# Kernel optimization log

Hardware: AMD Instinct MI355X
Metric: run time of the kernel (lower is better)

## Reference

```python
import jax, jax.numpy as jnp
import numpy as np
import math

EMBED_DIM = 1024
NUM_HEADS = 16
HEAD_DIM = EMBED_DIM // NUM_HEADS
B, S = 4, 2048


def setup_inputs() -> dict:
    key = jax.random.key(0)
    ks = jax.random.split(key, 12)
    sc = 1.0 / math.sqrt(EMBED_DIM)
    inp = {
        'query': jax.random.normal(ks[0], (B, S, EMBED_DIM), jnp.float32),
        'key': jax.random.normal(ks[1], (B, S, EMBED_DIM), jnp.float32),
        'value': jax.random.normal(ks[2], (B, S, EMBED_DIM), jnp.float32),
        # causal mask: 1 = attend, 0 = masked (matches masked_fill(attn_mask == 0, -inf))
        'attn_mask': jnp.tril(jnp.ones((S, S), jnp.int32)),
        'Wq': jax.random.normal(ks[3], (EMBED_DIM, EMBED_DIM), jnp.float32) * sc,
        'bq': jax.random.normal(ks[4], (EMBED_DIM,), jnp.float32) * sc,
        'Wk': jax.random.normal(ks[5], (EMBED_DIM, EMBED_DIM), jnp.float32) * sc,
        'bk': jax.random.normal(ks[6], (EMBED_DIM,), jnp.float32) * sc,
        'Wv': jax.random.normal(ks[7], (EMBED_DIM, EMBED_DIM), jnp.float32) * sc,
        'bv': jax.random.normal(ks[8], (EMBED_DIM,), jnp.float32) * sc,
        'Wo': jax.random.normal(ks[9], (EMBED_DIM, EMBED_DIM), jnp.float32) * sc,
        'bo': jax.random.normal(ks[10], (EMBED_DIM,), jnp.float32) * sc,
    }
    return inp


def reference(query, key, value, attn_mask, Wq, bq, Wk, bk, Wv, bv, Wo, bo):
    b, s, _ = query.shape
    # torch nn.Linear: x @ W.T + b
    q = (query @ Wq.T + bq).reshape(b, s, NUM_HEADS, HEAD_DIM)
    k = (key @ Wk.T + bk).reshape(b, s, NUM_HEADS, HEAD_DIM)
    v = (value @ Wv.T + bv).reshape(b, s, NUM_HEADS, HEAD_DIM)
    scores = jnp.einsum('bqhd,bkhd->bhqk', q, k) / math.sqrt(HEAD_DIM)
    neg_inf = jnp.asarray(-jnp.inf, scores.dtype)
    scores = jnp.where(attn_mask[None, None, :, :] == 0, neg_inf, scores)
    attn = jax.nn.softmax(scores, axis=-1)
    # dropout is identity in eval mode
    out = jnp.einsum('bhqk,bkhd->bqhd', attn, v).reshape(b, s, EMBED_DIM)
    return out @ Wo.T + bo
```

## Files before the change

kernel.cpp:

```cpp
#include <hip/hip_runtime.h>
#include <math.h>


#define EMBED 1024
#define SEQ   2048
#define NH    16
#define HD    64
#define QSCALE 0.18033688011112042f

typedef __attribute__((ext_vector_type(4))) float f32x4;
typedef __attribute__((ext_vector_type(8))) short s16x8;
typedef __attribute__((ext_vector_type(4))) short s16x4;
typedef __attribute__((ext_vector_type(4))) unsigned int u32x4;
typedef __attribute__((ext_vector_type(2))) unsigned int u32x2;

#define GLDS16(gp, lp) __builtin_amdgcn_global_load_lds( \
    (const __attribute__((address_space(1))) void*)(gp), \
    (__attribute__((address_space(3))) void*)(lp), 16, 0, 0)

__device__ __forceinline__ unsigned short f2bf(float f) {
    unsigned int u = __builtin_bit_cast(unsigned int, f);
    u += 0x7fffu + ((u >> 16) & 1u);
    return (unsigned short)(u >> 16);
}
__device__ __forceinline__ unsigned int pkbf(float lo, float hi) {
    return __builtin_amdgcn_perm(__builtin_bit_cast(unsigned int, hi),
                                 __builtin_bit_cast(unsigned int, lo),
                                 0x07060302u);
}

struct CvtArgs { const float* s[4]; unsigned short* d[4]; };
__global__ void cvt_w(CvtArgs ca)
{
    const float* in = ca.s[blockIdx.y];
    unsigned short* out = ca.d[blockIdx.y];
    int i = blockIdx.x * 256 + threadIdx.x;
    f32x4 v = *(const f32x4*)(in + (size_t)i * 4);
    s16x4 p;
    p[0] = (short)f2bf(v[0]); p[1] = (short)f2bf(v[1]);
    p[2] = (short)f2bf(v[2]); p[3] = (short)f2bf(v[3]);
    *(s16x4*)(out + (size_t)i * 4) = p;
}

struct ProjArgs {
    const float* X[3];
    const unsigned short* W[3];
    const float* Bz[3];
    unsigned short* Oz[3];
};
__global__ void __launch_bounds__(256)
gemm_qkv(ProjArgs pa)
{
    __shared__ float Af[128 * 64];
    __shared__ unsigned short Bb[128 * 64];
    const int z = blockIdx.z;
    const float* X = pa.X[z];
    const unsigned short* Wb = pa.W[z];
    const float* bias = pa.Bz[z];
    unsigned short* Out = pa.Oz[z];
    const float scale = (z == 0) ? QSCALE : 1.0f;
    const int tid = threadIdx.x, lane = tid & 63, wv = tid >> 6;
    const int g = lane >> 4, c = lane & 15;
    const int wx = wv & 1, wy = wv >> 1;
    const int bm0 = blockIdx.x * 128, bn0 = blockIdx.y * 128;

    f32x4 acc[4][4];
#pragma unroll
    for (int i = 0; i < 4; ++i)
#pragma unroll
        for (int n = 0; n < 4; ++n) acc[i][n] = f32x4{0.f, 0.f, 0.f, 0.f};

    for (int k0 = 0; k0 < EMBED; k0 += 64) {
        __syncthreads();
#pragma unroll
        for (int cc = 0; cc < 8; ++cc) {
            int li = cc * 256 + tid;
            int row = li >> 4, ch = (li & 15) ^ (row & 15);
            GLDS16(X + (size_t)(bm0 + row) * EMBED + k0 + ch * 4,
                   Af + cc * 1024 + wv * 256);
        }
#pragma unroll
        for (int cc = 0; cc < 4; ++cc) {
            int li = cc * 256 + tid;
            int row = li >> 3, ch = (li & 7) ^ (row & 7);
            GLDS16(Wb + (size_t)(bn0 + row) * EMBED + k0 + ch * 8,
                   Bb + cc * 2048 + wv * 512);
        }
        __syncthreads();
#pragma unroll
        for (int ks = 0; ks < 2; ++ks) {
            const int ia0 = ((ks * 8 + g * 2) ^ c) * 4;
            const int ia1 = ((ks * 8 + g * 2 + 1) ^ c) * 4;
            const int ib  = ((ks * 4 + g) ^ (c & 7)) * 8;
            s16x8 af[4], bfr[4];
#pragma unroll
            for (int i = 0; i < 4; ++i) {
                const float* ap = &Af[(wy * 64 + i * 16 + c) * 64];
                f32x4 a0 = *(const f32x4*)(ap + ia0);
                f32x4 a1 = *(const f32x4*)(ap + ia1);
                u32x4 t;
                t[0] = pkbf(a0[0], a0[1]); t[1] = pkbf(a0[2], a0[3]);
                t[2] = pkbf(a1[0], a1[1]); t[3] = pkbf(a1[2], a1[3]);
                af[i] = __builtin_bit_cast(s16x8, t);
            }
#pragma unroll
            for (int n = 0; n < 4; ++n)
                bfr[n] = *(const s16x8*)(&Bb[(wx * 64 + n * 16 + c) * 64 + ib]);
#pragma unroll
            for (int i = 0; i < 4; ++i)
#pragma unroll
                for (int n = 0; n < 4; ++n)
                    acc[i][n] = __builtin_amdgcn_mfma_f32_16x16x32_bf16(af[i], bfr[n], acc[i][n], 0, 0, 0);
        }
    }
    if (z < 2) {
#pragma unroll
        for (int i = 0; i < 4; ++i) {
            int m0 = bm0 + wy * 64 + i * 16 + g * 4;
            int bb = m0 >> 11, s0 = m0 & 2047;
#pragma unroll
            for (int n = 0; n < 4; ++n) {
                int ncol = bn0 + wx * 64 + n * 16 + c;
                float bv = bias[ncol];
                int hh = ncol >> 6, dd = ncol & 63;
                size_t base = (((size_t)bb * NH + hh) * SEQ + s0) * HD + dd;
#pragma unroll
                for (int r = 0; r < 4; ++r)
                    Out[base + (size_t)r * HD] = f2bf((acc[i][n][r] + bv) * scale);
            }
        }
    } else {
#pragma unroll
        for (int i = 0; i < 4; ++i) {
            int m0 = bm0 + wy * 64 + i * 16 + g * 4;
            int bb = m0 >> 11, s0 = m0 & 2047;
#pragma unroll
            for (int n = 0; n < 4; ++n) {
                int ncol = bn0 + wx * 64 + n * 16 + c;
                float bv = bias[ncol];
                int hh = ncol >> 6, dd = ncol & 63;
                s16x4 pk;
#pragma unroll
                for (int r = 0; r < 4; ++r) pk[r] = (short)f2bf(acc[i][n][r] + bv);
                *(s16x4*)(&Out[(((size_t)bb * NH + hh) * HD + dd) * SEQ + s0]) = pk;
            }
        }
    }
}

__global__ void __launch_bounds__(256)
gemm_out(const unsigned short* __restrict__ Xb, const unsigned short* __restrict__ Wb,
         const float* __restrict__ bias, float* __restrict__ Out)
{
    __shared__ unsigned short Ab[128 * 64];
    __shared__ unsigned short Bb[128 * 64];
    const int tid = threadIdx.x;
    const int lane = tid & 63, wv = tid >> 6;
    const int g = lane >> 4, c = lane & 15;
    const int wx = wv & 1, wy = wv >> 1;
    const int bm0 = blockIdx.x * 128, bn0 = blockIdx.y * 128;

    f32x4 acc[4][4];
#pragma unroll
    for (int i = 0; i < 4; ++i)
#pragma unroll
        for (int n = 0; n < 4; ++n) acc[i][n] = f32x4{0.f, 0.f, 0.f, 0.f};

    for (int k0 = 0; k0 < EMBED; k0 += 64) {
        __syncthreads();
#pragma unroll
        for (int cc = 0; cc < 4; ++cc) {
            int li = cc * 256 + tid;
            int row = li >> 3, ch = (li & 7) ^ (row & 7);
            GLDS16(Xb + (size_t)(bm0 + row) * EMBED + k0 + ch * 8,
                   Ab + cc * 2048 + wv * 512);
        }
#pragma unroll
        for (int cc = 0; cc < 4; ++cc) {
            int li = cc * 256 + tid;
            int row = li >> 3, ch = (li & 7) ^ (row & 7);
            GLDS16(Wb + (size_t)(bn0 + row) * EMBED + k0 + ch * 8,
                   Bb + cc * 2048 + wv * 512);
        }
        __syncthreads();
#pragma unroll
        for (int ks = 0; ks < 2; ++ks) {
            const int ib = ((ks * 4 + g) ^ (c & 7)) * 8;
            s16x8 af[4], bfr[4];
#pragma unroll
            for (int i = 0; i < 4; ++i)
                af[i] = *(const s16x8*)(&Ab[(wy * 64 + i * 16 + c) * 64 + ib]);
#pragma unroll
            for (int n = 0; n < 4; ++n)
                bfr[n] = *(const s16x8*)(&Bb[(wx * 64 + n * 16 + c) * 64 + ib]);
#pragma unroll
            for (int i = 0; i < 4; ++i)
#pragma unroll
                for (int n = 0; n < 4; ++n)
                    acc[i][n] = __builtin_amdgcn_mfma_f32_16x16x32_bf16(af[i], bfr[n], acc[i][n], 0, 0, 0);
        }
    }
#pragma unroll
    for (int i = 0; i < 4; ++i) {
#pragma unroll
        for (int n = 0; n < 4; ++n) {
            int ncol = bn0 + wx * 64 + n * 16 + c;
            float bv = bias[ncol];
#pragma unroll
            for (int r = 0; r < 4; ++r) {
                int m = bm0 + wy * 64 + i * 16 + g * 4 + r;
                Out[(size_t)m * EMBED + ncol] = acc[i][n][r] + bv;
            }
        }
    }
}

__global__ void __launch_bounds__(256)
attn_fwd(const unsigned short* __restrict__ Qb, const unsigned short* __restrict__ Kb,
         const unsigned short* __restrict__ Vg, unsigned short* __restrict__ Ob)
{
    __shared__ unsigned short Kt[2][64 * 64];
    __shared__ unsigned short Vt[2][64 * 64];
    __shared__ unsigned int   Pb[4][16 * 36];
    const int tid = threadIdx.x, lane = tid & 63, wv = tid >> 6;
    const int g = lane >> 4, c = lane & 15;
    const int h = blockIdx.y, b = blockIdx.z;
    const size_t bh = (size_t)b * NH + h;
    const unsigned short* K0 = Kb + bh * SEQ * HD;
    const unsigned short* V0 = Vg + bh * HD * SEQ;
    unsigned int* Pw = &Pb[wv][0];
    const int x0 = (g ^ (c & 7)) * 8;
    const int x1 = ((4 + g) ^ (c & 7)) * 8;
    const int li0 = tid, li1 = 256 + tid;
    const int kr0 = (li0 >> 3) * HD + (((li0 & 7) ^ ((li0 >> 3) & 7)) << 3);
    const int kr1 = (li1 >> 3) * HD + (((li1 & 7) ^ ((li1 >> 3) & 7)) << 3);
    const int vr0 = (li0 >> 3) * SEQ + (((li0 & 7) ^ ((li0 >> 3) & 7)) << 3);
    const int vr1 = (li1 >> 3) * SEQ + (((li1 & 7) ^ ((li1 >> 3) & 7)) << 3);

    for (int part = 0; part < 2; ++part) {
        const int qt = part ? blockIdx.x : (SEQ / 64 - 1 - blockIdx.x);
        const unsigned short* Qp = Qb + (bh * SEQ + qt * 64 + wv * 16) * HD;
        s16x8 qf0 = *(const s16x8*)(Qp + c * HD + g * 8);
        s16x8 qf1 = *(const s16x8*)(Qp + c * HD + 32 + g * 8);
        f32x4 o[4];
#pragma unroll
        for (int dt = 0; dt < 4; ++dt) o[dt] = f32x4{0.f, 0.f, 0.f, 0.f};
        float m_run = -INFINITY, l_run = 0.f;

        __syncthreads();
        {
            const unsigned short* Kg = K0;
            GLDS16(Kg + kr0, &Kt[0][0] + wv * 512);
            GLDS16(Kg + kr1, &Kt[0][2048] + wv * 512);
            GLDS16(V0 + vr0, &Vt[0][0] + wv * 512);
            GLDS16(V0 + vr1, &Vt[0][2048] + wv * 512);
        }

        for (int kt = 0; kt <= qt; ++kt) {
            __syncthreads();
            const int cur = kt & 1;
            if (kt < qt) {
                const int nxt = cur ^ 1;
                const unsigned short* Kg = K0 + (size_t)(kt + 1) * 64 * HD;
                GLDS16(Kg + kr0, &Kt[nxt][0] + wv * 512);
                GLDS16(Kg + kr1, &Kt[nxt][2048] + wv * 512);
                const unsigned short* Vp = V0 + (kt + 1) * 64;
                GLDS16(Vp + vr0, &Vt[nxt][0] + wv * 512);
                GLDS16(Vp + vr1, &Vt[nxt][2048] + wv * 512);
            }
            const unsigned short* Kc = &Kt[cur][0];
            const unsigned short* Vc = &Vt[cur][0];

            const int ntmax = (kt == qt) ? wv : 3;
            f32x4 sc[4];
#pragma unroll
            for (int nt = 0; nt < 4; ++nt) {
                if (nt <= ntmax) {
                    f32x4 a = f32x4{0.f, 0.f, 0.f, 0.f};
                    s16x8 kf0 = *(const s16x8*)(&Kc[(nt * 16 + c) * 64 + x0]);
                    s16x8 kf1 = *(const s16x8*)(&Kc[(nt * 16 + c) * 64 + x1]);
                    a = __builtin_amdgcn_mfma_f32_16x16x32_bf16(kf0, qf0, a, 0, 0, 0);
                    a = __builtin_amdgcn_mfma_f32_16x16x32_bf16(kf1, qf1, a, 0, 0, 0);
                    sc[nt] = a;
                } else {
                    sc[nt] = f32x4{-INFINITY, -INFINITY, -INFINITY, -INFINITY};
                }
            }
            if (kt == qt) {
#pragma unroll
                for (int nt = 0; nt < 4; ++nt)
#pragma unroll
                    for (int r = 0; r < 4; ++r)
                        if (nt * 16 + g * 4 + r > wv * 16 + c) sc[nt][r] = -INFINITY;
            }
            float mloc = -INFINITY;
#pragma unroll
            for (int nt = 0; nt < 4; ++nt)
                mloc = fmaxf(mloc, fmaxf(fmaxf(sc[nt][0], sc[nt][1]),
                                         fmaxf(sc[nt][2], sc[nt][3])));
            mloc = fmaxf(mloc, __shfl_xor(mloc, 16));
            mloc = fmaxf(mloc, __shfl_xor(mloc, 32));
            if (__any(mloc > m_run)) {
                float mnew = fmaxf(m_run, mloc);
                float alpha = __builtin_amdgcn_exp2f(m_run - mnew);
                m_run = mnew;
                l_run *= alpha;
                float av[4];
#pragma unroll
                for (int r = 0; r < 4; ++r) av[r] = __shfl(alpha, g * 4 + r, 16);
#pragma unroll
                for (int dt = 0; dt < 4; ++dt)
#pragma unroll
                    for (int r = 0; r < 4; ++r) o[dt][r] *= av[r];
            }
            float rs = 0.f;
#pragma unroll
            for (int nt = 0; nt < 4; ++nt)
#pragma unroll
                for (int r = 0; r < 4; ++r) {
                    float p = __builtin_amdgcn_exp2f(sc[nt][r] - m_run);
                    sc[nt][r] = p;
                    rs += p;
                }
            rs += __shfl_xor(rs, 16);
            rs += __shfl_xor(rs, 32);
            l_run += rs;
#pragma unroll
            for (int nt = 0; nt < 4; ++nt) {
                u32x2 w;
                w[0] = pkbf(sc[nt][0], sc[nt][1]);
                w[1] = pkbf(sc[nt][2], sc[nt][3]);
                *(u32x2*)(&Pw[c * 36 + nt * 8 + g * 2]) = w;
            }
#pragma unroll
            for (int kc = 0; kc < 2; ++kc) {
                s16x8 pf = *(const s16x8*)(&Pw[c * 36 + kc * 16 + g * 4]);
                const int xv = kc ? x1 : x0;
#pragma unroll
                for (int dt = 0; dt < 4; ++dt) {
                    s16x8 vf = *(const s16x8*)(&Vc[(dt * 16 + c) * 64 + xv]);
                    o[dt] = __builtin_amdgcn_mfma_f32_16x16x32_bf16(pf, vf, o[dt], 0, 0, 0);
                }
            }
        }
        float linv = 1.0f / l_run;
        float lv[4];
#pragma unroll
        for (int r = 0; r < 4; ++r) lv[r] = __shfl(linv, g * 4 + r, 16);
#pragma unroll
        for (int r = 0; r < 4; ++r) {
            int srow = qt * 64 + wv * 16 + g * 4 + r;
            size_t base = ((size_t)b * SEQ + srow) * EMBED + h * HD;
#pragma unroll
            for (int dt = 0; dt < 4; ++dt)
                Ob[base + dt * 16 + c] = f2bf(o[dt][r] * lv[r]);
        }
    }
}

extern "C" void kernel_launch(void* const* d_in, const int* in_sizes, int n_in,
                              void* d_out, int out_size, void* d_ws, size_t ws_size,
                              hipStream_t stream)
{
    (void)in_sizes; (void)n_in; (void)out_size; (void)ws_size;
    const float* Xq = (const float*)d_in[0];
    const float* Xk = (const float*)d_in[1];
    const float* Xv = (const float*)d_in[2];
    const float* Wq = (const float*)d_in[4];
    const float* bq = (const float*)d_in[5];
    const float* Wk = (const float*)d_in[6];
    const float* bk = (const float*)d_in[7];
    const float* Wv = (const float*)d_in[8];
    const float* bv = (const float*)d_in[9];
    const float* Wo = (const float*)d_in[10];
    const float* bo = (const float*)d_in[11];
    float* Out = (float*)d_out;

    unsigned short* ws = (unsigned short*)d_ws;
    unsigned short* wqb = ws;
    unsigned short* wkb = wqb + 1048576;
    unsigned short* wvb = wkb + 1048576;
    unsigned short* wob = wvb + 1048576;
    unsigned short* Qb  = wob + 1048576;
    unsigned short* Kb  = Qb + 8388608;
    unsigned short* Vb  = Kb + 8388608;
    unsigned short* Ax  = Vb + 8388608;

    CvtArgs ca;
    ca.s[0] = Wq; ca.s[1] = Wk; ca.s[2] = Wv; ca.s[3] = Wo;
    ca.d[0] = wqb; ca.d[1] = wkb; ca.d[2] = wvb; ca.d[3] = wob;
    cvt_w<<<dim3(1024, 4), 256, 0, stream>>>(ca);

    ProjArgs pa;
    pa.X[0] = Xq; pa.X[1] = Xk; pa.X[2] = Xv;
    pa.W[0] = wqb; pa.W[1] = wkb; pa.W[2] = wvb;
    pa.Bz[0] = bq; pa.Bz[1] = bk; pa.Bz[2] = bv;
    pa.Oz[0] = Qb; pa.Oz[1] = Kb; pa.Oz[2] = Vb;
    gemm_qkv<<<dim3(64, 8, 3), 256, 0, stream>>>(pa);

    attn_fwd<<<dim3(16, NH, 4), 256, 0, stream>>>(Qb, Kb, Vb, Ax);

    gemm_out<<<dim3(64, 8), 256, 0, stream>>>(Ax, wob, bo, Out);
}
```

Baseline: 350.9 us.

## Pre-convert activations to bf16, swap GEMM grid order, unpair attention blocks

Activations X are now converted to bf16 in one combined conversion kernel along with the weights. The QKV GEMM therefore streams bf16 A tiles instead of fp32 tiles converted in-loop, which halves A-side LDS and global traffic in that GEMM. The GEMM grids are transposed so consecutive blocks share the same M rows across N tiles, aiming at better L2 reuse of A. The attention kernel drops the paired long/short q-tile scheme for one q-tile per block, launched in reverse order for load balance. The cost is an extra full pass over the inputs, using d_out and Ax as scratch buffers, and potentially worse tail balance in attention.

```diff
diff --git a/kernel.cpp b/kernel.cpp
--- a/kernel.cpp
+++ b/kernel.cpp
@@ -11,7 +11,6 @@
 typedef __attribute__((ext_vector_type(4))) float f32x4;
 typedef __attribute__((ext_vector_type(8))) short s16x8;
 typedef __attribute__((ext_vector_type(4))) short s16x4;
-typedef __attribute__((ext_vector_type(4))) unsigned int u32x4;
 typedef __attribute__((ext_vector_type(2))) unsigned int u32x2;
 
 #define GLDS16(gp, lp) __builtin_amdgcn_global_load_lds( \
@@ -29,21 +28,23 @@
                                  0x07060302u);
 }
 
-struct CvtArgs { const float* s[4]; unsigned short* d[4]; };
-__global__ void cvt_w(CvtArgs ca)
-{
-    const float* in = ca.s[blockIdx.y];
-    unsigned short* out = ca.d[blockIdx.y];
+struct CvtArgs { const float* s[7]; unsigned short* d[7]; };
+__global__ void cvt_all(CvtArgs ca)
+{
+    const int y = blockIdx.y;
+    const int n4 = (y < 3) ? (1 << 21) : (1 << 18);
     int i = blockIdx.x * 256 + threadIdx.x;
-    f32x4 v = *(const f32x4*)(in + (size_t)i * 4);
-    s16x4 p;
-    p[0] = (short)f2bf(v[0]); p[1] = (short)f2bf(v[1]);
-    p[2] = (short)f2bf(v[2]); p[3] = (short)f2bf(v[3]);
-    *(s16x4*)(out + (size_t)i * 4) = p;
+    if (i < n4) {
+        f32x4 v = *(const f32x4*)(ca.s[y] + (size_t)i * 4);
+        s16x4 p;
+        p[0] = (short)f2bf(v[0]); p[1] = (short)f2bf(v[1]);
+        p[2] = (short)f2bf(v[2]); p[3] = (short)f2bf(v[3]);
+        *(s16x4*)(ca.d[y] + (size_t)i * 4) = p;
+    }
 }
 
 struct ProjArgs {
-    const float* X[3];
+    const unsigned short* X[3];
     const unsigned short* W[3];
     const float* Bz[3];
     unsigned short* Oz[3];
@@ -51,10 +52,10 @@
 __global__ void __launch_bounds__(256)
 gemm_qkv(ProjArgs pa)
 {
-    __shared__ float Af[128 * 64];
+    __shared__ unsigned short Ab[128 * 64];
     __shared__ unsigned short Bb[128 * 64];
     const int z = blockIdx.z;
-    const float* X = pa.X[z];
+    const unsigned short* Xb = pa.X[z];
     const unsigned short* Wb = pa.W[z];
     const float* bias = pa.Bz[z];
     unsigned short* Out = pa.Oz[z];
@@ -62,7 +63,7 @@
     const int tid = threadIdx.x, lane = tid & 63, wv = tid >> 6;
     const int g = lane >> 4, c = lane & 15;
     const int wx = wv & 1, wy = wv >> 1;
-    const int bm0 = blockIdx.x * 128, bn0 = blockIdx.y * 128;
+    const int bn0 = blockIdx.x * 128, bm0 = blockIdx.y * 128;
 
     f32x4 acc[4][4];
 #pragma unroll
@@ -73,11 +74,11 @@
     for (int k0 = 0; k0 < EMBED; k0 += 64) {
         __syncthreads();
 #pragma unroll
-        for (int cc = 0; cc < 8; ++cc) {
+        for (int cc = 0; cc < 4; ++cc) {
             int li = cc * 256 + tid;
-            int row = li >> 4, ch = (li & 15) ^ (row & 15);
-            GLDS16(X + (size_t)(bm0 + row) * EMBED + k0 + ch * 4,
-                   Af + cc * 1024 + wv * 256);
+            int row = li >> 3, ch = (li & 7) ^ (row & 7);
+            GLDS16(Xb + (size_t)(bm0 + row) * EMBED + k0 + ch * 8,
+                   Ab + cc * 2048 + wv * 512);
         }
 #pragma unroll
         for (int cc = 0; cc < 4; ++cc) {
@@ -89,20 +90,11 @@
         __syncthreads();
 #pragma unroll
         for (int ks = 0; ks < 2; ++ks) {
-            const int ia0 = ((ks * 8 + g * 2) ^ c) * 4;
-            const int ia1 = ((ks * 8 + g * 2 + 1) ^ c) * 4;
-            const int ib  = ((ks * 4 + g) ^ (c & 7)) * 8;
+            const int ib = ((ks * 4 + g) ^ (c & 7)) * 8;
             s16x8 af[4], bfr[4];
 #pragma unroll
-            for (int i = 0; i < 4; ++i) {
-                const float* ap = &Af[(wy * 64 + i * 16 + c) * 64];
-                f32x4 a0 = *(const f32x4*)(ap + ia0);
-                f32x4 a1 = *(const f32x4*)(ap + ia1);
-                u32x4 t;
-                t[0] = pkbf(a0[0], a0[1]); t[1] = pkbf(a0[2], a0[3]);
-                t[2] = pkbf(a1[0], a1[1]); t[3] = pkbf(a1[2], a1[3]);
-                af[i] = __builtin_bit_cast(s16x8, t);
-            }
+            for (int i = 0; i < 4; ++i)
+                af[i] = *(const s16x8*)(&Ab[(wy * 64 + i * 16 + c) * 64 + ib]);
 #pragma unroll
             for (int n = 0; n < 4; ++n)
                 bfr[n] = *(const s16x8*)(&Bb[(wx * 64 + n * 16 + c) * 64 + ib]);
@@ -158,7 +150,7 @@
     const int lane = tid & 63, wv = tid >> 6;
     const int g = lane >> 4, c = lane & 15;
     const int wx = wv & 1, wy = wv >> 1;
-    const int bm0 = blockIdx.x * 128, bn0 = blockIdx.y * 128;
+    const int bn0 = blockIdx.x * 128, bm0 = blockIdx.y * 128;
 
     f32x4 acc[4][4];
 #pragma unroll
@@ -237,124 +229,120 @@
     const int vr0 = (li0 >> 3) * SEQ + (((li0 & 7) ^ ((li0 >> 3) & 7)) << 3);
     const int vr1 = (li1 >> 3) * SEQ + (((li1 & 7) ^ ((li1 >> 3) & 7)) << 3);
 
-    for (int part = 0; part < 2; ++part) {
-        const int qt = part ? blockIdx.x : (SEQ / 64 - 1 - blockIdx.x);
-        const unsigned short* Qp = Qb + (bh * SEQ + qt * 64 + wv * 16) * HD;
-        s16x8 qf0 = *(const s16x8*)(Qp + c * HD + g * 8);
-        s16x8 qf1 = *(const s16x8*)(Qp + c * HD + 32 + g * 8);
-        f32x4 o[4];
-#pragma unroll
-        for (int dt = 0; dt < 4; ++dt) o[dt] = f32x4{0.f, 0.f, 0.f, 0.f};
-        float m_run = -INFINITY, l_run = 0.f;
-
-        __syncthreads();
-        {
-            const unsigned short* Kg = K0;
-            GLDS16(Kg + kr0, &Kt[0][0] + wv * 512);
-            GLDS16(Kg + kr1, &Kt[0][2048] + wv * 512);
-            GLDS16(V0 + vr0, &Vt[0][0] + wv * 512);
-            GLDS16(V0 + vr1, &Vt[0][2048] + wv * 512);
-        }
-
-        for (int kt = 0; kt <= qt; ++kt) {
-            __syncthreads();
-            const int cur = kt & 1;
-            if (kt < qt) {
-                const int nxt = cur ^ 1;
-                const unsigned short* Kg = K0 + (size_t)(kt + 1) * 64 * HD;
-                GLDS16(Kg + kr0, &Kt[nxt][0] + wv * 512);
-                GLDS16(Kg + kr1, &Kt[nxt][2048] + wv * 512);
-                const unsigned short* Vp = V0 + (kt + 1) * 64;
-                GLDS16(Vp + vr0, &Vt[nxt][0] + wv * 512);
-                GLDS16(Vp + vr1, &Vt[nxt][2048] + wv * 512);
-            }
-            const unsigned short* Kc = &Kt[cur][0];
-            const unsigned short* Vc = &Vt[cur][0];
-
-            const int ntmax = (kt == qt) ? wv : 3;
-            f32x4 sc[4];
-#pragma unroll
-            for (int nt = 0; nt < 4; ++nt) {
-                if (nt <= ntmax) {
-                    f32x4 a = f32x4{0.f, 0.f, 0.f, 0.f};
-                    s16x8 kf0 = *(const s16x8*)(&Kc[(nt * 16 + c) * 64 + x0]);
-                    s16x8 kf1 = *(const s16x8*)(&Kc[(nt * 16 + c) * 64 + x1]);
-                    a = __builtin_amdgcn_mfma_f32_16x16x32_bf16(kf0, qf0, a, 0, 0, 0);
-                    a = __builtin_amdgcn_mfma_f32_16x16x32_bf16(kf1, qf1, a, 0, 0, 0);
-                    sc[nt] = a;
-                } else {
-                    sc[nt] = f32x4{-INFINITY, -INFINITY, -INFINITY, -INFINITY};
-                }
-            }
-            if (kt == qt) {
-#pragma unroll
-                for (int nt = 0; nt < 4; ++nt)
-#pragma unroll
-                    for (int r = 0; r < 4; ++r)
-                        if (nt * 16 + g * 4 + r > wv * 16 + c) sc[nt][r] = -INFINITY;
-            }
-            float mloc = -INFINITY;
+    const int qt = (SEQ / 64 - 1) - blockIdx.x;
+    const unsigned short* Qp = Qb + (bh * SEQ + qt * 64 + wv * 16) * HD;
+    s16x8 qf0 = *(const s16x8*)(Qp + c * HD + g * 8);
+    s16x8 qf1 = *(const s16x8*)(Qp + c * HD + 32 + g * 8);
+    f32x4 o[4];
+#pragma unroll
+    for (int dt = 0; dt < 4; ++dt) o[dt] = f32x4{0.f, 0.f, 0.f, 0.f};
+    float m_run = -INFINITY, l_run = 0.f;
+
+    {
+        GLDS16(K0 + kr0, &Kt[0][0] + wv * 512);
+        GLDS16(K0 + kr1, &Kt[0][2048] + wv * 512);
+        GLDS16(V0 + vr0, &Vt[0][0] + wv * 512);
+        GLDS16(V0 + vr1, &Vt[0][2048] + wv * 512);
+    }
+
+    for (int kt = 0; kt <= qt; ++kt) {
+        __syncthreads();
+        const int cur = kt & 1;
+        if (kt < qt) {
+            const int nxt = cur ^ 1;
+            const unsigned short* Kg = K0 + (size_t)(kt + 1) * 64 * HD;
+            GLDS16(Kg + kr0, &Kt[nxt][0] + wv * 512);
+            GLDS16(Kg + kr1, &Kt[nxt][2048] + wv * 512);
+            const unsigned short* Vp = V0 + (kt + 1) * 64;
+            GLDS16(Vp + vr0, &Vt[nxt][0] + wv * 512);
+            GLDS16(Vp + vr1, &Vt[nxt][2048] + wv * 512);
+        }
+        const unsigned short* Kc = &Kt[cur][0];
+        const unsigned short* Vc = &Vt[cur][0];
+
+        const int ntmax = (kt == qt) ? wv : 3;
+        f32x4 sc[4];
+#pragma unroll
+        for (int nt = 0; nt < 4; ++nt) {
+            if (nt <= ntmax) {
+                f32x4 a = f32x4{0.f, 0.f, 0.f, 0.f};
+                s16x8 kf0 = *(const s16x8*)(&Kc[(nt * 16 + c) * 64 + x0]);
+                s16x8 kf1 = *(const s16x8*)(&Kc[(nt * 16 + c) * 64 + x1]);
+                a = __builtin_amdgcn_mfma_f32_16x16x32_bf16(kf0, qf0, a, 0, 0, 0);
+                a = __builtin_amdgcn_mfma_f32_16x16x32_bf16(kf1, qf1, a, 0, 0, 0);
+                sc[nt] = a;
+            } else {
+                sc[nt] = f32x4{-INFINITY, -INFINITY, -INFINITY, -INFINITY};
+            }
+        }
+        if (kt == qt) {
 #pragma unroll
             for (int nt = 0; nt < 4; ++nt)
-                mloc = fmaxf(mloc, fmaxf(fmaxf(sc[nt][0], sc[nt][1]),
-                                         fmaxf(sc[nt][2], sc[nt][3])));
-            mloc = fmaxf(mloc, __shfl_xor(mloc, 16));
-            mloc = fmaxf(mloc, __shfl_xor(mloc, 32));
-            if (__any(mloc > m_run)) {
-                float mnew = fmaxf(m_run, mloc);
-                float alpha = __builtin_amdgcn_exp2f(m_run - mnew);
-                m_run = mnew;
-                l_run *= alpha;
-                float av[4];
-#pragma unroll
-                for (int r = 0; r < 4; ++r) av[r] = __shfl(alpha, g * 4 + r, 16);
-#pragma unroll
-                for (int dt = 0; dt < 4; ++dt)
-#pragma unroll
-                    for (int r = 0; r < 4; ++r) o[dt][r] *= av[r];
-            }
-            float rs = 0.f;
-#pragma unroll
-            for (int nt = 0; nt < 4; ++nt)
-#pragma unroll
-                for (int r = 0; r < 4; ++r) {
-                    float p = __builtin_amdgcn_exp2f(sc[nt][r] - m_run);
-                    sc[nt][r] = p;
-                    rs += p;
-                }
-            rs += __shfl_xor(rs, 16);
-            rs += __shfl_xor(rs, 32);
-            l_run += rs;
-#pragma unroll
-            for (int nt = 0; nt < 4; ++nt) {
-                u32x2 w;
-                w[0] = pkbf(sc[nt][0], sc[nt][1]);
-                w[1] = pkbf(sc[nt][2], sc[nt][3]);
-                *(u32x2*)(&Pw[c * 36 + nt * 8 + g * 2]) = w;
-            }
-#pragma unroll
-            for (int kc = 0; kc < 2; ++kc) {
-                s16x8 pf = *(const s16x8*)(&Pw[c * 36 + kc * 16 + g * 4]);
-                const int xv = kc ? x1 : x0;
-#pragma unroll
-                for (int dt = 0; dt < 4; ++dt) {
-                    s16x8 vf = *(const s16x8*)(&Vc[(dt * 16 + c) * 64 + xv]);
-                    o[dt] = __builtin_amdgcn_mfma_f32_16x16x32_bf16(pf, vf, o[dt], 0, 0, 0);
-                }
-            }
-        }
-        float linv = 1.0f / l_run;
-        float lv[4];
-#pragma unroll
-        for (int r = 0; r < 4; ++r) lv[r] = __shfl(linv, g * 4 + r, 16);
-#pragma unroll
-        for (int r = 0; r < 4; ++r) {
-            int srow = qt * 64 + wv * 16 + g * 4 + r;
-            size_t base = ((size_t)b * SEQ + srow) * EMBED + h * HD;
+#pragma unroll
+                for (int r = 0; r < 4; ++r)
+                    if (nt * 16 + g * 4 + r > wv * 16 + c) sc[nt][r] = -INFINITY;
+        }
+        float mloc = -INFINITY;
+#pragma unroll
+        for (int nt = 0; nt < 4; ++nt)
+            mloc = fmaxf(mloc, fmaxf(fmaxf(sc[nt][0], sc[nt][1]),
+                                     fmaxf(sc[nt][2], sc[nt][3])));
+        mloc = fmaxf(mloc, __shfl_xor(mloc, 16));
+        mloc = fmaxf(mloc, __shfl_xor(mloc, 32));
+        if (__any(mloc > m_run)) {
+            float mnew = fmaxf(m_run, mloc);
+            float alpha = __builtin_amdgcn_exp2f(m_run - mnew);
+            m_run = mnew;
+            l_run *= alpha;
+            float av[4];
+#pragma unroll
+            for (int r = 0; r < 4; ++r) av[r] = __shfl(alpha, g * 4 + r, 16);
 #pragma unroll
             for (int dt = 0; dt < 4; ++dt)
-                Ob[base + dt * 16 + c] = f2bf(o[dt][r] * lv[r]);
-        }
+#pragma unroll
+                for (int r = 0; r < 4; ++r) o[dt][r] *= av[r];
+        }
+        float rs = 0.f;
+#pragma unroll
+        for (int nt = 0; nt < 4; ++nt)
+#pragma unroll
+            for (int r = 0; r < 4; ++r) {
+                float p = __builtin_amdgcn_exp2f(sc[nt][r] - m_run);
+                sc[nt][r] = p;
+                rs += p;
+            }
+        rs += __shfl_xor(rs, 16);
+        rs += __shfl_xor(rs, 32);
+        l_run += rs;
+#pragma unroll
+        for (int nt = 0; nt < 4; ++nt) {
+            u32x2 w;
+            w[0] = pkbf(sc[nt][0], sc[nt][1]);
+            w[1] = pkbf(sc[nt][2], sc[nt][3]);
+            *(u32x2*)(&Pw[c * 36 + nt * 8 + g * 2]) = w;
+        }
+#pragma unroll
+        for (int kc = 0; kc < 2; ++kc) {
+            s16x8 pf = *(const s16x8*)(&Pw[c * 36 + kc * 16 + g * 4]);
+            const int xv = kc ? x1 : x0;
+#pragma unroll
+            for (int dt = 0; dt < 4; ++dt) {
+                s16x8 vf = *(const s16x8*)(&Vc[(dt * 16 + c) * 64 + xv]);
+                o[dt] = __builtin_amdgcn_mfma_f32_16x16x32_bf16(pf, vf, o[dt], 0, 0, 0);
+            }
+        }
+    }
+    float linv = 1.0f / l_run;
+    float lv[4];
+#pragma unroll
+    for (int r = 0; r < 4; ++r) lv[r] = __shfl(linv, g * 4 + r, 16);
+#pragma unroll
+    for (int r = 0; r < 4; ++r) {
+        int srow = qt * 64 + wv * 16 + g * 4 + r;
+        size_t base = ((size_t)b * SEQ + srow) * EMBED + h * HD;
+#pragma unroll
+        for (int dt = 0; dt < 4; ++dt)
+            Ob[base + dt * 16 + c] = f2bf(o[dt][r] * lv[r]);
     }
 }
 
@@ -385,20 +373,25 @@
     unsigned short* Kb  = Qb + 8388608;
     unsigned short* Vb  = Kb + 8388608;
     unsigned short* Ax  = Vb + 8388608;
+    unsigned short* Xqb = (unsigned short*)d_out;
+    unsigned short* Xkb = Xqb + 8388608;
+    unsigned short* Xvb = Ax;
 
     CvtArgs ca;
-    ca.s[0] = Wq; ca.s[1] = Wk; ca.s[2] = Wv; ca.s[3] = Wo;
-    ca.d[0] = wqb; ca.d[1] = wkb; ca.d[2] = wvb; ca.d[3] = wob;
-    cvt_w<<<dim3(1024, 4), 256, 0, stream>>>(ca);
+    ca.s[0] = Xq; ca.s[1] = Xk; ca.s[2] = Xv;
+    ca.s[3] = Wq; ca.s[4] = Wk; ca.s[5] = Wv; ca.s[6] = Wo;
+    ca.d[0] = Xqb; ca.d[1] = Xkb; ca.d[2] = Xvb;
+    ca.d[3] = wqb; ca.d[4] = wkb; ca.d[5] = wvb; ca.d[6] = wob;
+    cvt_all<<<dim3(8192, 7), 256, 0, stream>>>(ca);
 
     ProjArgs pa;
-    pa.X[0] = Xq; pa.X[1] = Xk; pa.X[2] = Xv;
+    pa.X[0] = Xqb; pa.X[1] = Xkb; pa.X[2] = Xvb;
     pa.W[0] = wqb; pa.W[1] = wkb; pa.W[2] = wvb;
     pa.Bz[0] = bq; pa.Bz[1] = bk; pa.Bz[2] = bv;
     pa.Oz[0] = Qb; pa.Oz[1] = Kb; pa.Oz[2] = Vb;
-    gemm_qkv<<<dim3(64, 8, 3), 256, 0, stream>>>(pa);
-
-    attn_fwd<<<dim3(16, NH, 4), 256, 0, stream>>>(Qb, Kb, Vb, Ax);
-
-    gemm_out<<<dim3(64, 8), 256, 0, stream>>>(Ax, wob, bo, Out);
-}
+    gemm_qkv<<<dim3(8, 64, 3), 256, 0, stream>>>(pa);
+
+    attn_fwd<<<dim3(32, NH, 4), 256, 0, stream>>>(Qb, Kb, Vb, Ax);
+
+    gemm_out<<<dim3(8, 64), 256, 0, stream>>>(Ax, wob, bo, Out);
+}
```

After: 410.7 us. 17.0% more time.
